# Kernel tuning notes

Hardware: AMD Instinct MI355X
Metric: run time of the kernel (lower is better)

Reference implementation:

```python
import jax, jax.numpy as jnp
import numpy as np

FEAT_DIM, M, K, D = 1024, 32, 256, 32
B = 8192
ALPHA = 1.0
BN_EPS = 1e-5
NORM_EPS = 1e-12  # F.normalize eps


def _l2_normalize(v, axis=-1):
    # matches torch F.normalize: v / max(||v||, eps)
    n = jnp.sqrt(jnp.sum(v * v, axis=axis, keepdims=True))
    return v / jnp.maximum(n, NORM_EPS)


def setup_inputs() -> dict:
    key = jax.random.key(0)
    kx, kc = jax.random.split(key)
    x = jax.random.normal(kx, (B, FEAT_DIM), dtype=jnp.float32)
    # xavier-uniform init over (M,K,D) then per-codeword L2 normalization (as in __init__)
    limit = float(np.sqrt(6.0 / (K + D)))
    C_k = jax.random.uniform(kc, (M, K, D), dtype=jnp.float32, minval=-limit, maxval=limit)
    C_k = _l2_normalize(C_k, axis=-1)
    return {"x": x, "C_k": C_k}


def reference(x, C_k):
    Bn = x.shape[0]
    x_ = x.reshape(Bn, M, D)                       # (B, M, D)
    x_norm_ = _l2_normalize(x_, axis=-1)           # per-subspace normalize
    x_normalized = x_norm_.reshape(Bn, FEAT_DIM)

    # per-subspace similarity: (B, M, K)
    sims = jnp.einsum('bmd,mkd->bmk', x_norm_, C_k)

    # BatchNorm1d(M, affine=False) in training mode: normalize per channel m over (B, K)
    mean = jnp.mean(sims, axis=(0, 2), keepdims=True)
    var = jnp.mean(jnp.square(sims - mean), axis=(0, 2), keepdims=True)  # biased var
    sims = (sims - mean) / jnp.sqrt(var + BN_EPS)

    # hard assignment + codeword gather (C_v == C_k in VQ mode)
    hard_codes = jnp.argmax(sims, axis=-1)                     # (B, M) int
    x_hat_hard_ = C_k[jnp.arange(M)[None, :], hard_codes]      # (B, M, D)
    x_hat_hard = x_hat_hard_.reshape(Bn, FEAT_DIM)

    # soft assignment (mask_topK is None)
    soft_codes = jax.nn.softmax(sims * ALPHA, axis=-1)         # (B, M, K)

    # straight-through: value = x_hat_hard, grad flows through x_normalized
    x_hat = x_normalized - jax.lax.stop_gradient(x_normalized - x_hat_hard)

    # pq_detach_opt == 'features'
    reg_loss = jnp.sum(jnp.square(jax.lax.stop_gradient(x_normalized) - x_hat_hard), axis=-1)  # (B,)

    return (x_hat, hard_codes, soft_codes, x_normalized, reg_loss)
```

## Files before the change

### kernel.cpp

```cpp
#include <hip/hip_runtime.h>
#include <cmath>

#define FEAT_DIM 1024
#define MM 32
#define KK 256
#define DD 32
#define BB 8192

constexpr float BN_EPS = 1e-5f;

typedef float f32x4 __attribute__((ext_vector_type(4)));

__device__ __forceinline__ float wave_fsum(float v) {
    #pragma unroll
    for (int s = 32; s >= 1; s >>= 1) v += __shfl_xor(v, s);
    return v;
}

template <int CTRL, int RM = 0xf>
__device__ __forceinline__ float dppf(float v) {
    int r = __builtin_amdgcn_update_dpp(__builtin_bit_cast(int, v),
                                        __builtin_bit_cast(int, v),
                                        CTRL, RM, 0xf, false);
    return __builtin_bit_cast(float, r);
}
__device__ __forceinline__ float wave_dpp_max(float v) {
    v = fmaxf(v, dppf<0xB1>(v));
    v = fmaxf(v, dppf<0x4E>(v));
    v = fmaxf(v, dppf<0x141>(v));
    v = fmaxf(v, dppf<0x140>(v));
    v = fmaxf(v, dppf<0x142, 0xa>(v));
    v = fmaxf(v, dppf<0x143, 0xc>(v));
    return __builtin_bit_cast(float, __builtin_amdgcn_readlane(__builtin_bit_cast(int, v), 63));
}
__device__ __forceinline__ float wave_dpp_sum(float v) {
    v += dppf<0xB1>(v);
    v += dppf<0x4E>(v);
    v += dppf<0x141>(v);
    v += dppf<0x140>(v);
    v += dppf<0x142, 0xa>(v);
    v += dppf<0x143, 0xc>(v);
    return __builtin_bit_cast(float, __builtin_amdgcn_readlane(__builtin_bit_cast(int, v), 63));
}

__global__ void k_norm(const float* __restrict__ x, float* __restrict__ xn,
                       double* __restrict__ stats) {
    if (blockIdx.x == 0 && threadIdx.x < 2 * MM) stats[threadIdx.x] = 0.0;
    const int t = blockIdx.x * blockDim.x + threadIdx.x;
    float4 v = ((const float4*)x)[t];
    float ss = v.x*v.x + v.y*v.y + v.z*v.z + v.w*v.w;
    #pragma unroll
    for (int s = 1; s < 8; s <<= 1) ss += __shfl_xor(ss, s);
    const float r = 1.0f / fmaxf(sqrtf(ss), 1e-12f);
    float4 o = {v.x*r, v.y*r, v.z*r, v.w*r};
    ((float4*)xn)[t] = o;
}

__global__ void k_gram(const float* __restrict__ Ck, float* __restrict__ G,
                       float* __restrict__ S) {
    __shared__ float CT[DD][KK + 4];
    const int m = blockIdx.x, part = blockIdx.y;
    const int t = threadIdx.x, wid = t >> 6, lane = t & 63;
    const float4* cp = (const float4*)(Ck + ((size_t)m * KK + t) * DD);
    #pragma unroll
    for (int i = 0; i < 8; ++i) {
        float4 v = cp[i];
        CT[4*i+0][t] = v.x; CT[4*i+1][t] = v.y;
        CT[4*i+2][t] = v.z; CT[4*i+3][t] = v.w;
    }
    __syncthreads();
    #pragma unroll 1
    for (int ei = 0; ei < 32; ++ei) {
        const int e = part * 128 + wid * 32 + ei;
        const int i = e >> 5, j = e & 31;
        float acc = 0.f;
        #pragma unroll
        for (int c4 = 0; c4 < 4; ++c4)
            acc = fmaf(CT[i][lane + 64*c4], CT[j][lane + 64*c4], acc);
        acc = wave_fsum(acc);
        if (lane == 0) G[((size_t)m * DD + i) * DD + j] = acc;
    }
    if (part == 0 && wid == 0) {
        #pragma unroll 1
        for (int d = 0; d < DD; ++d) {
            float a = 0.f;
            #pragma unroll
            for (int c4 = 0; c4 < 4; ++c4) a += CT[d][lane + 64*c4];
            a = wave_fsum(a);
            if (lane == 0) S[m * DD + d] = a;
        }
    }
}

__global__ void k_stats2(const float* __restrict__ xn, const float* __restrict__ G,
                         const float* __restrict__ S, double* __restrict__ stats) {
    const int m = blockIdx.x;
    const int b = blockIdx.y * 256 + threadIdx.x;
    float xv[DD];
    {
        const float4* xp = (const float4*)(xn + (size_t)b * FEAT_DIM + m * DD);
        #pragma unroll
        for (int i = 0; i < 8; ++i) {
            float4 v = xp[i];
            xv[4*i+0]=v.x; xv[4*i+1]=v.y; xv[4*i+2]=v.z; xv[4*i+3]=v.w;
        }
    }
    const float4* Gp = (const float4*)(G + (size_t)m * DD * DD);
    const float*  Sp = S + m * DD;
    float q = 0.f, s = 0.f;
    #pragma unroll 4
    for (int i = 0; i < DD; ++i) {
        float y = 0.f;
        #pragma unroll
        for (int jv = 0; jv < 8; ++jv) {
            float4 g = Gp[i * 8 + jv];
            y = fmaf(g.x, xv[4*jv+0], y); y = fmaf(g.y, xv[4*jv+1], y);
            y = fmaf(g.z, xv[4*jv+2], y); y = fmaf(g.w, xv[4*jv+3], y);
        }
        q = fmaf(y, xv[i], q);
    }
    #pragma unroll
    for (int i = 0; i < DD; ++i) s = fmaf(Sp[i], xv[i], s);
    q = wave_fsum(q); s = wave_fsum(s);
    __shared__ float lq[4], ls[4];
    const int wid = threadIdx.x >> 6, lane = threadIdx.x & 63;
    if (lane == 0) { lq[wid] = q; ls[wid] = s; }
    __syncthreads();
    if (threadIdx.x == 0) {
        atomicAdd(&stats[2*m],   (double)((ls[0]+ls[1])+(ls[2]+ls[3])));
        atomicAdd(&stats[2*m+1], (double)((lq[0]+lq[1])+(lq[2]+lq[3])));
    }
}

template <int BT>
__global__ __launch_bounds__(256, 2)
void k_main(const float* __restrict__ xn, const float* __restrict__ Ck,
            const double* __restrict__ stats,
            float* __restrict__ hard, float* __restrict__ soft,
            float* __restrict__ part) {
    const int m = blockIdx.x;
    const int wid = threadIdx.x >> 6, lane = threadIdx.x & 63;

    const double Ninv = 1.0 / ((double)BB * (double)KK);
    const double mu  = stats[2*m] * Ninv;
    const double var = stats[2*m+1] * Ninv - mu * mu;
    const float rstd = (float)(1.0 / sqrt(var + (double)BN_EPS));
    const float c1 = rstd * 1.4426950408889634f;

    float c[4][DD];
    #pragma unroll
    for (int j = 0; j < 4; ++j) {
        const float4* cp = (const float4*)(Ck + ((size_t)m * KK + 4*lane + j) * DD);
        #pragma unroll
        for (int i = 0; i < 8; ++i) {
            float4 v = cp[i];
            c[j][4*i+0]=v.x; c[j][4*i+1]=v.y; c[j][4*i+2]=v.z; c[j][4*i+3]=v.w;
        }
    }

    const int b_base = blockIdx.y * (4 * BT) + wid;

    auto loadslice = [&](float4 (&q)[8], int b) {
        const int bu = __builtin_amdgcn_readfirstlane(b);
        const float4* xp = (const float4*)(xn + (size_t)bu * FEAT_DIM + m * DD);
        #pragma unroll
        for (int i = 0; i < 8; ++i) q[i] = xp[i];
    };

    auto process = [&](const float4 (&q)[8], int b) {
        float d0=0.f, d1=0.f, d2=0.f, d3=0.f;
        #pragma unroll
        for (int i = 0; i < 8; ++i) {
            const float4 q4 = q[i];
            d0 = fmaf(q4.x, c[0][4*i+0], d0); d0 = fmaf(q4.y, c[0][4*i+1], d0);
            d0 = fmaf(q4.z, c[0][4*i+2], d0); d0 = fmaf(q4.w, c[0][4*i+3], d0);
            d1 = fmaf(q4.x, c[1][4*i+0], d1); d1 = fmaf(q4.y, c[1][4*i+1], d1);
            d1 = fmaf(q4.z, c[1][4*i+2], d1); d1 = fmaf(q4.w, c[1][4*i+3], d1);
            d2 = fmaf(q4.x, c[2][4*i+0], d2); d2 = fmaf(q4.y, c[2][4*i+1], d2);
            d2 = fmaf(q4.z, c[2][4*i+2], d2); d2 = fmaf(q4.w, c[2][4*i+3], d2);
            d3 = fmaf(q4.x, c[3][4*i+0], d3); d3 = fmaf(q4.y, c[3][4*i+1], d3);
            d3 = fmaf(q4.z, c[3][4*i+2], d3); d3 = fmaf(q4.w, c[3][4*i+3], d3);
        }

        const float p0 = exp2f(d0 * c1);
        const float p1 = exp2f(d1 * c1);
        const float p2 = exp2f(d2 * c1);
        const float p3 = exp2f(d3 * c1);

        const float mx = wave_dpp_max(fmaxf(fmaxf(d0, d1), fmaxf(d2, d3)));
        const unsigned long long m0 = __ballot(d0 == mx);
        const unsigned long long m1 = __ballot(d1 == mx);
        const unsigned long long m2 = __ballot(d2 == mx);
        const unsigned long long m3 = __ballot(d3 == mx);
        const int k0 = m0 ? 4*__builtin_ctzll(m0)+0 : 0x7fffffff;
        const int k1 = m1 ? 4*__builtin_ctzll(m1)+1 : 0x7fffffff;
        const int k2 = m2 ? 4*__builtin_ctzll(m2)+2 : 0x7fffffff;
        const int k3 = m3 ? 4*__builtin_ctzll(m3)+3 : 0x7fffffff;
        const int bi = min(min(k0, k1), min(k2, k3));

        const float tot = wave_dpp_sum((p0 + p1) + (p2 + p3));
        const float inv = __builtin_amdgcn_rcpf(tot);

        f32x4 o = {p0*inv, p1*inv, p2*inv, p3*inv};
        __builtin_nontemporal_store(o, (f32x4*)(soft + ((size_t)b * MM + m) * KK) + lane);
        if (lane == 0) {
            hard[(size_t)b * MM + m] = (float)bi;
            part[(size_t)m * BB + b] = 2.f - 2.f * mx;
        }
    };

    float4 A[8], Bv[8];
    loadslice(A, b_base);
    #pragma unroll 1
    for (int it = 0; it < BT; it += 2) {
        loadslice(Bv, b_base + 4 * (it + 1));
        process(A, b_base + 4 * it);
        if (it + 2 < BT) loadslice(A, b_base + 4 * (it + 2));
        process(Bv, b_base + 4 * (it + 1));
    }
}

__global__ void k_xhat(const float* __restrict__ Ck, const float* __restrict__ hard,
                       float* __restrict__ xhat) {
    const int t = blockIdx.x * 256 + threadIdx.x;
    const int i = t & 7, bm = t >> 3;
    const int m = bm & (MM - 1);
    const int k = (int)hard[bm];
    f32x4 cw = ((const f32x4*)(Ck + ((size_t)m * KK + k) * DD))[i];
    __builtin_nontemporal_store(cw, ((f32x4*)xhat) + (size_t)bm * 8 + i);
}

__global__ void k_regsum(const float* __restrict__ part, float* __restrict__ reg) {
    const int b = blockIdx.x * 256 + threadIdx.x;
    float a = 0.f;
    #pragma unroll
    for (int mm = 0; mm < MM; ++mm) a += part[(size_t)mm * BB + b];
    reg[b] = a;
}

extern "C" void kernel_launch(void* const* d_in, const int* in_sizes, int n_in,
                              void* d_out, int out_size, void* d_ws, size_t ws_size,
                              hipStream_t stream) {
    const float* x  = (const float*)d_in[0];
    const float* Ck = (const float*)d_in[1];

    float* out   = (float*)d_out;
    float* xhat  = out;
    float* hard  = xhat  + (size_t)BB * FEAT_DIM;
    float* soft  = hard  + (size_t)BB * MM;
    float* xnorm = soft  + (size_t)BB * MM * KK;
    float* reg   = xnorm + (size_t)BB * FEAT_DIM;

    double* stats = (double*)d_ws;
    float* partb  = (float*)d_ws + 256;
    float* Gbuf = soft;
    float* Sbuf = soft + (size_t)MM * DD * DD;

    k_norm<<<(BB * FEAT_DIM / 4) / 256, 256, 0, stream>>>(x, xnorm, stats);
    k_gram<<<dim3(MM, 8), 256, 0, stream>>>(Ck, Gbuf, Sbuf);
    k_stats2<<<dim3(MM, BB / 256), 256, 0, stream>>>(xnorm, Gbuf, Sbuf, stats);
    constexpr int BT = 32;
    k_main<BT><<<dim3(MM, BB / (4 * BT)), 256, 0, stream>>>(xnorm, Ck, stats, hard, soft, partb);
    k_xhat<<<(BB * MM * 8) / 256, 256, 0, stream>>>(Ck, hard, xhat);
    k_regsum<<<BB / 256, 256, 0, stream>>>(partb, reg);
}
```

Before: 162.4 us.

## Stage codebook and x slices in LDS, process 8 rows per wave iteration

k_main no longer keeps 128 codebook floats per thread in registers. It stages the per-subspace codebook in LDS and streams x rows into a double-buffered LDS tile using global_load_lds with manual vmcnt waits. Each wave now computes 8 batch rows per iteration, so every codebook fragment read from LDS is reused across those rows. This cuts register pressure and overlaps the global loads with compute, at the cost of LDS bandwidth, 40KB of shared memory per block and fragile hand-written waitcnt ordering.

```diff
diff --git a/kernel.cpp b/kernel.cpp
--- a/kernel.cpp
+++ b/kernel.cpp
@@ -132,14 +132,16 @@
     }
 }
 
-template <int BT>
-__global__ __launch_bounds__(256, 2)
+#define NB  8
+#define BTI 8
+__global__ __launch_bounds__(256)
 void k_main(const float* __restrict__ xn, const float* __restrict__ Ck,
             const double* __restrict__ stats,
             float* __restrict__ hard, float* __restrict__ soft,
             float* __restrict__ part) {
+    __shared__ float lds[10240];
     const int m = blockIdx.x;
-    const int wid = threadIdx.x >> 6, lane = threadIdx.x & 63;
+    const int t = threadIdx.x, w = t >> 6, lane = t & 63;
 
     const double Ninv = 1.0 / ((double)BB * (double)KK);
     const double mu  = stats[2*m] * Ninv;
@@ -147,41 +149,28 @@
     const float rstd = (float)(1.0 / sqrt(var + (double)BN_EPS));
     const float c1 = rstd * 1.4426950408889634f;
 
-    float c[4][DD];
-    #pragma unroll
-    for (int j = 0; j < 4; ++j) {
-        const float4* cp = (const float4*)(Ck + ((size_t)m * KK + 4*lane + j) * DD);
-        #pragma unroll
-        for (int i = 0; i < 8; ++i) {
-            float4 v = cp[i];
-            c[j][4*i+0]=v.x; c[j][4*i+1]=v.y; c[j][4*i+2]=v.z; c[j][4*i+3]=v.w;
-        }
-    }
-
-    const int b_base = blockIdx.y * (4 * BT) + wid;
-
-    auto loadslice = [&](float4 (&q)[8], int b) {
-        const int bu = __builtin_amdgcn_readfirstlane(b);
-        const float4* xp = (const float4*)(xn + (size_t)bu * FEAT_DIM + m * DD);
-        #pragma unroll
-        for (int i = 0; i < 8; ++i) q[i] = xp[i];
+    {
+        const f32x4* cg = (const f32x4*)(Ck + ((size_t)m * KK + t) * DD);
+        const int j = t & 3, l = t >> 2;
+        #pragma unroll
+        for (int i = 0; i < 8; ++i)
+            *(f32x4*)&lds[((j * 8 + i) * 64 + l) * 4] = cg[i];
+    }
+    __syncthreads();
+
+    const int wbase = blockIdx.y * (4 * NB * BTI) + w * (NB * BTI);
+    float* xlds = &lds[8192 + w * 512];
+
+    auto stage = [&](int it) {
+        const int b = wbase + it * NB + (lane >> 3);
+        const float* gp = xn + (size_t)b * FEAT_DIM + m * DD + (lane & 7) * 4;
+        __builtin_amdgcn_global_load_lds(
+            (const __attribute__((address_space(1))) unsigned int*)gp,
+            (__attribute__((address_space(3))) unsigned int*)&xlds[(it & 1) * 256],
+            16, 0, 0);
     };
 
-    auto process = [&](const float4 (&q)[8], int b) {
-        float d0=0.f, d1=0.f, d2=0.f, d3=0.f;
-        #pragma unroll
-        for (int i = 0; i < 8; ++i) {
-            const float4 q4 = q[i];
-            d0 = fmaf(q4.x, c[0][4*i+0], d0); d0 = fmaf(q4.y, c[0][4*i+1], d0);
-            d0 = fmaf(q4.z, c[0][4*i+2], d0); d0 = fmaf(q4.w, c[0][4*i+3], d0);
-            d1 = fmaf(q4.x, c[1][4*i+0], d1); d1 = fmaf(q4.y, c[1][4*i+1], d1);
-            d1 = fmaf(q4.z, c[1][4*i+2], d1); d1 = fmaf(q4.w, c[1][4*i+3], d1);
-            d2 = fmaf(q4.x, c[2][4*i+0], d2); d2 = fmaf(q4.y, c[2][4*i+1], d2);
-            d2 = fmaf(q4.z, c[2][4*i+2], d2); d2 = fmaf(q4.w, c[2][4*i+3], d2);
-            d3 = fmaf(q4.x, c[3][4*i+0], d3); d3 = fmaf(q4.y, c[3][4*i+1], d3);
-            d3 = fmaf(q4.z, c[3][4*i+2], d3); d3 = fmaf(q4.w, c[3][4*i+3], d3);
-        }
-
+    auto FINISH = [&](float d0, float d1, float d2, float d3, int b) {
         const float p0 = exp2f(d0 * c1);
         const float p1 = exp2f(d1 * c1);
         const float p2 = exp2f(d2 * c1);
@@ -209,14 +198,51 @@
         }
     };
 
-    float4 A[8], Bv[8];
-    loadslice(A, b_base);
+    stage(0);
     #pragma unroll 1
-    for (int it = 0; it < BT; it += 2) {
-        loadslice(Bv, b_base + 4 * (it + 1));
-        process(A, b_base + 4 * it);
-        if (it + 2 < BT) loadslice(A, b_base + 4 * (it + 2));
-        process(Bv, b_base + 4 * (it + 1));
+    for (int it = 0; it < BTI; ++it) {
+        if (it == 0) asm volatile("s_waitcnt vmcnt(0)" ::: "memory");
+        else         asm volatile("s_waitcnt vmcnt(24)" ::: "memory");
+        __builtin_amdgcn_sched_barrier(0);
+        if (it + 1 < BTI) stage(it + 1);
+        __builtin_amdgcn_sched_barrier(0);
+
+        const float* xb = &xlds[(it & 1) * 256];
+        float acc[NB][4];
+        #pragma unroll
+        for (int s = 0; s < NB; ++s) {
+            acc[s][0]=0.f; acc[s][1]=0.f; acc[s][2]=0.f; acc[s][3]=0.f;
+        }
+        #pragma unroll
+        for (int i = 0; i < 8; ++i) {
+            f32x4 cc0 = *(const f32x4*)&lds[((0 * 8 + i) * 64 + lane) * 4];
+            f32x4 cc1 = *(const f32x4*)&lds[((1 * 8 + i) * 64 + lane) * 4];
+            f32x4 cc2 = *(const f32x4*)&lds[((2 * 8 + i) * 64 + lane) * 4];
+            f32x4 cc3 = *(const f32x4*)&lds[((3 * 8 + i) * 64 + lane) * 4];
+            #pragma unroll
+            for (int s = 0; s < NB; ++s) {
+                const f32x4 xv = *(const f32x4*)&xb[s * 32 + i * 4];
+                acc[s][0] = fmaf(xv[0], cc0[0], acc[s][0]);
+                acc[s][0] = fmaf(xv[1], cc0[1], acc[s][0]);
+                acc[s][0] = fmaf(xv[2], cc0[2], acc[s][0]);
+                acc[s][0] = fmaf(xv[3], cc0[3], acc[s][0]);
+                acc[s][1] = fmaf(xv[0], cc1[0], acc[s][1]);
+                acc[s][1] = fmaf(xv[1], cc1[1], acc[s][1]);
+                acc[s][1] = fmaf(xv[2], cc1[2], acc[s][1]);
+                acc[s][1] = fmaf(xv[3], cc1[3], acc[s][1]);
+                acc[s][2] = fmaf(xv[0], cc2[0], acc[s][2]);
+                acc[s][2] = fmaf(xv[1], cc2[1], acc[s][2]);
+                acc[s][2] = fmaf(xv[2], cc2[2], acc[s][2]);
+                acc[s][2] = fmaf(xv[3], cc2[3], acc[s][2]);
+                acc[s][3] = fmaf(xv[0], cc3[0], acc[s][3]);
+                acc[s][3] = fmaf(xv[1], cc3[1], acc[s][3]);
+                acc[s][3] = fmaf(xv[2], cc3[2], acc[s][3]);
+                acc[s][3] = fmaf(xv[3], cc3[3], acc[s][3]);
+            }
+        }
+        #pragma unroll
+        for (int s = 0; s < NB; ++s)
+            FINISH(acc[s][0], acc[s][1], acc[s][2], acc[s][3], wbase + it * NB + s);
     }
 }
 
@@ -259,8 +285,7 @@
     k_norm<<<(BB * FEAT_DIM / 4) / 256, 256, 0, stream>>>(x, xnorm, stats);
     k_gram<<<dim3(MM, 8), 256, 0, stream>>>(Ck, Gbuf, Sbuf);
     k_stats2<<<dim3(MM, BB / 256), 256, 0, stream>>>(xnorm, Gbuf, Sbuf, stats);
-    constexpr int BT = 32;
-    k_main<BT><<<dim3(MM, BB / (4 * BT)), 256, 0, stream>>>(xnorm, Ck, stats, hard, soft, partb);
+    k_main<<<dim3(MM, BB / 256), 256, 0, stream>>>(xnorm, Ck, stats, hard, soft, partb);
     k_xhat<<<(BB * MM * 8) / 256, 256, 0, stream>>>(Ck, hard, xhat);
     k_regsum<<<BB / 256, 256, 0, stream>>>(partb, reg);
 }
```

After: 216.2 us. 33.2% more time.
